# Optimization experiments

Measured on AMD Instinct MI355X. Metric: run time of the kernel, lower is better.

The kernel has to match this reference:

```python
import jax, jax.numpy as jnp
import numpy as np

NEG_SLOPE = 0.2   # GATConv default leaky_relu slope
BN_EPS = 1e-5
N, D, H, DH, E, BS = 49152, 512, 8, 64, 131072, 12
N_LAYERS = 5  # conv6 exists in __init__ but is never called in forward


def setup_inputs() -> dict:
    key = jax.random.key(0)
    ks = jax.random.split(key, 12)
    s = 0.05
    x = jax.random.normal(ks[0], (N, D), jnp.float32)
    edge_index = jax.random.randint(ks[1], (2, E), 0, N, jnp.int64)
    Ws = jax.random.normal(ks[2], (N_LAYERS, D, H * DH), jnp.float32) * s
    Asrc = jax.random.normal(ks[3], (N_LAYERS, H, DH), jnp.float32) * s
    Adst = jax.random.normal(ks[4], (N_LAYERS, H, DH), jnp.float32) * s
    Bconv = jax.random.normal(ks[5], (N_LAYERS, H * DH), jnp.float32) * s
    Gamma = jnp.ones((N_LAYERS, D), jnp.float32)
    Beta = jnp.zeros((N_LAYERS, D), jnp.float32)
    Wl = jax.random.normal(ks[6], (D, 1), jnp.float32) * s
    bl = jnp.zeros((1,), jnp.float32)
    return {"x": x, "edge_index": edge_index, "Ws": Ws, "Asrc": Asrc,
            "Adst": Adst, "Bconv": Bconv, "Gamma": Gamma, "Beta": Beta,
            "Wl": Wl, "bl": bl, "bs": BS}


def _gat_conv(x, src, dst, W, a_src, a_dst, b):
    n = x.shape[0]
    h = (x @ W).reshape(n, H, DH)                      # [N,H,DH]
    al_s = jnp.einsum('nhd,hd->nh', h, a_src)          # [N,H]
    al_d = jnp.einsum('nhd,hd->nh', h, a_dst)
    e = jax.nn.leaky_relu(al_s[src] + al_d[dst], NEG_SLOPE)  # [Etot,H]
    # segment softmax over incoming edges of each dst node
    m = jax.ops.segment_max(e, dst, num_segments=n)
    p = jnp.exp(e - m[dst])
    z = jax.ops.segment_sum(p, dst, num_segments=n)
    alpha = p / (z[dst] + 1e-16)
    out = jax.ops.segment_sum(alpha[:, :, None] * h[src], dst, num_segments=n)
    return out.reshape(n, H * DH) + b


def _batch_norm(x, gamma, beta):
    mu = x.mean(0)
    var = x.var(0)  # biased, as torch BN uses for normalization
    return (x - mu) * jax.lax.rsqrt(var + BN_EPS) * gamma + beta


def reference(x, edge_index, Ws, Asrc, Adst, Bconv, Gamma, Beta, Wl, bl, bs):
    n = x.shape[0]
    loops = jnp.arange(n, dtype=edge_index.dtype)      # add_self_loops=True
    src = jnp.concatenate([edge_index[0], loops])
    dst = jnp.concatenate([edge_index[1], loops])
    for i in range(N_LAYERS):
        x = _gat_conv(x, src, dst, Ws[i], Asrc[i], Adst[i], Bconv[i])
        x = jax.nn.relu(_batch_norm(x, Gamma[i], Beta[i]))
    w = x @ Wl + bl                                    # [N,1]
    return w.reshape(bs, -1)
```

## Files before the change

### kernel.cpp

```cpp
#include <hip/hip_runtime.h>
#include <cstdint>

#define N_NODES 49152
#define DIM 512
#define NH 8
#define DHEAD 64
#define NE 131072
#define ETOT (NE + N_NODES)
#define NLAYERS 5
#define AGG_NODES 32
#define AGG_BLOCKS (N_NODES / AGG_NODES)

typedef short short8 __attribute__((ext_vector_type(8)));
typedef float floatx4 __attribute__((ext_vector_type(4)));

__device__ __forceinline__ float bf2f(unsigned short v) {
  union { unsigned int u; float f; } x; x.u = ((unsigned int)v) << 16; return x.f;
}
__device__ __forceinline__ unsigned short f2bf(float f) {
  union { float f; unsigned int u; } x; x.f = f;
  unsigned int r = x.u + 0x7fffu + ((x.u >> 16) & 1u);
  return (unsigned short)(r >> 16);
}
__device__ __forceinline__ void async_load16(const void* g, void* l) {
  __builtin_amdgcn_global_load_lds((const __attribute__((address_space(1))) void*)g,
                                   (__attribute__((address_space(3))) void*)l, 16, 0, 0);
}

__global__ __launch_bounds__(256) void convert_x_r7(const float* __restrict__ xf, unsigned short* __restrict__ xb)
{
  const size_t i = ((size_t)blockIdx.x * 256 + threadIdx.x) * 8;
  const float4 a = *(const float4*)&xf[i];
  const float4 b = *(const float4*)&xf[i + 4];
  unsigned int ov[4];
  ov[0] = (unsigned int)f2bf(a.x) | ((unsigned int)f2bf(a.y) << 16);
  ov[1] = (unsigned int)f2bf(a.z) | ((unsigned int)f2bf(a.w) << 16);
  ov[2] = (unsigned int)f2bf(b.x) | ((unsigned int)f2bf(b.y) << 16);
  ov[3] = (unsigned int)f2bf(b.z) | ((unsigned int)f2bf(b.w) << 16);
  *(uint4*)&xb[i] = *(const uint4*)ov;
}

__global__ void transpose_w_r7(const float* __restrict__ Ws, unsigned short* __restrict__ WT)
{
  __shared__ float tile[32][33];
  const int l  = blockIdx.z;
  const int nt = blockIdx.x * 32, kt = blockIdx.y * 32;
  const int tx = threadIdx.x & 31, ty = threadIdx.x >> 5;
  #pragma unroll
  for (int r = 0; r < 32; r += 8)
    tile[ty + r][tx] = Ws[(size_t)l*DIM*DIM + (size_t)(kt + ty + r)*DIM + nt + tx];
  __syncthreads();
  #pragma unroll
  for (int r = 0; r < 32; r += 8)
    WT[(size_t)l*DIM*DIM + (size_t)(nt + ty + r)*DIM + kt + tx] = f2bf(tile[tx][ty + r]);
}

__global__ void repack_edges_r7(const int* __restrict__ raw, int* __restrict__ eidx)
{
  const int i = blockIdx.x * 256 + threadIdx.x;
  bool is64 = true;
  #pragma unroll
  for (int j = 0; j < 16; j++) is64 = is64 && (raw[2*j + 1] == 0);
  int v;
  if (is64) v = (int)((const long long*)raw)[i];
  else      v = raw[i];
  eidx[i] = v;
}

__global__ void init_counts_r7(int* __restrict__ counts) {
  counts[blockIdx.x * 256 + threadIdx.x] = 1;
}
__global__ void hist_dst_r7(const int* __restrict__ eidx, int* __restrict__ counts) {
  const int i = blockIdx.x * 256 + threadIdx.x;
  atomicAdd(&counts[eidx[NE + i]], 1);
}
__global__ void scan_kernel_r7(const int* __restrict__ counts, int* __restrict__ offs, int* __restrict__ cursor)
{
  __shared__ int tot[1024];
  const int t = threadIdx.x;
  const int base = t * 48;
  int s = 0;
  for (int i = 0; i < 48; i++) s += counts[base + i];
  tot[t] = s;
  __syncthreads();
  for (int o = 1; o < 1024; o <<= 1) {
    int v = (t >= o) ? tot[t - o] : 0;
    __syncthreads();
    tot[t] += v;
    __syncthreads();
  }
  int run = tot[t] - s;
  for (int i = 0; i < 48; i++) {
    offs[base + i] = run;
    cursor[base + i] = run;
    run += counts[base + i];
  }
  if (t == 1023) offs[N_NODES] = tot[1023];
}
__global__ void scatter_edges_r7(const int* __restrict__ eidx, int* __restrict__ cursor, int* __restrict__ csrc)
{
  const int i = blockIdx.x * 256 + threadIdx.x;
  int s, d;
  if (i < NE) { s = eidx[i]; d = eidx[NE + i]; }
  else        { s = i - NE; d = s; }
  const int pos = atomicAdd(&cursor[d], 1);
  csrc[pos] = s;
}

__global__ __launch_bounds__(512, 4) void gemm_bt_r7(const unsigned short* __restrict__ A,
                                                     const unsigned short* __restrict__ BT,
                                                     const float* __restrict__ asrc,
                                                     const float* __restrict__ adst,
                                                     unsigned short* __restrict__ C,
                                                     float* __restrict__ als,
                                                     float* __restrict__ ald)
{
  __shared__ unsigned short As[128 * 64];
  __shared__ unsigned short Bs[256 * 64];
  const int m0 = blockIdx.x * 128;
  const int n0 = blockIdx.y * 256;
  const int tid = threadIdx.x;
  const int wv = tid >> 6, lane = tid & 63;
  const int wr = (wv & 1) * 64, wc = (wv >> 1) * 64;
  const int q = lane >> 4, c16 = lane & 15;
  const int arow = lane >> 3;
  const int acol = (lane & 7) * 8;

  floatx4 acc[4][4] = {};

  for (int k0 = 0; k0 < DIM; k0 += 64) {
    #pragma unroll
    for (int t = 0; t < 2; t++) {
      const int cb = wv * 2 + t;
      async_load16(A + (size_t)(m0 + cb*8 + arow)*DIM + k0 + acol, &As[cb * 512]);
    }
    #pragma unroll
    for (int t = 0; t < 4; t++) {
      const int cb = wv * 4 + t;
      async_load16(BT + (size_t)(n0 + cb*8 + arow)*DIM + k0 + acol, &Bs[cb * 512]);
    }
    __syncthreads();
    #pragma unroll
    for (int kk = 0; kk < 64; kk += 32) {
      short8 aF[4], bF[4];
      #pragma unroll
      for (int mt = 0; mt < 4; mt++)
        aF[mt] = *(const short8*)&As[(wr + mt*16 + c16) * 64 + kk + q*8];
      #pragma unroll
      for (int nt = 0; nt < 4; nt++)
        bF[nt] = *(const short8*)&Bs[(wc + nt*16 + c16) * 64 + kk + q*8];
      #pragma unroll
      for (int mt = 0; mt < 4; mt++)
        #pragma unroll
        for (int nt = 0; nt < 4; nt++)
          acc[mt][nt] = __builtin_amdgcn_mfma_f32_16x16x32_bf16(aF[mt], bF[nt], acc[mt][nt], 0, 0, 0);
    }
    __syncthreads();
  }
  #pragma unroll
  for (int mt = 0; mt < 4; mt++) {
    #pragma unroll
    for (int nt = 0; nt < 4; nt++) {
      const int col = n0 + wc + nt*16 + c16;
      #pragma unroll
      for (int r = 0; r < 4; r++) {
        const int row = m0 + wr + mt*16 + q*4 + r;
        C[(size_t)row * DIM + col] = f2bf(acc[mt][nt][r]);
      }
    }
  }
  const int head = 4 * blockIdx.y + (wc >> 6);
  float as_[4], ad_[4];
  #pragma unroll
  for (int nt = 0; nt < 4; nt++) {
    const int d = nt * 16 + c16;
    as_[nt] = asrc[head * DHEAD + d];
    ad_[nt] = adst[head * DHEAD + d];
  }
  #pragma unroll
  for (int mt = 0; mt < 4; mt++) {
    #pragma unroll
    for (int r = 0; r < 4; r++) {
      float ss = 0.f, sd = 0.f;
      #pragma unroll
      for (int nt = 0; nt < 4; nt++) {
        ss += acc[mt][nt][r] * as_[nt];
        sd += acc[mt][nt][r] * ad_[nt];
      }
      #pragma unroll
      for (int msk = 1; msk <= 8; msk <<= 1) {
        ss += __shfl_xor(ss, msk, 64);
        sd += __shfl_xor(sd, msk, 64);
      }
      if (c16 == 0) {
        const int row = m0 + wr + mt*16 + q*4 + r;
        als[row * NH + head] = ss;
        ald[row * NH + head] = sd;
      }
    }
  }
}

__global__ __launch_bounds__(256) void gat_agg_r7(const unsigned short* __restrict__ Hm,
    const float* __restrict__ als, const float* __restrict__ ald,
    const int* __restrict__ offs, const int* __restrict__ csrc,
    const float* __restrict__ bconv, unsigned short* __restrict__ Xout,
    float* __restrict__ ps, float* __restrict__ pq)
{
  __shared__ float red[4][1024];
  const int wv = threadIdx.x >> 6, lane = threadIdx.x & 63;
  const int hd = lane >> 3;
  const float4 bA = ((const float4*)(bconv + (size_t)lane * 8))[0];
  const float4 bB = ((const float4*)(bconv + (size_t)lane * 8))[1];
  const float barr[8] = {bA.x, bA.y, bA.z, bA.w, bB.x, bB.y, bB.z, bB.w};
  float cs[8] = {}, cq[8] = {};

  for (int i = 0; i < 8; i++) {
    const int node = blockIdx.x * AGG_NODES + wv * 8 + i;
    const float aldv = ald[node * NH + hd];
    const int e0 = offs[node], e1 = offs[node + 1];
    float m = -1e30f, z = 0.f;
    float acc[8] = {};
    for (int e = e0; e < e1; e++) {
      const int s = csrc[e];
      float lg = als[s * NH + hd] + aldv;
      lg = lg > 0.f ? lg : 0.2f * lg;
      const float mn = fmaxf(m, lg);
      const float sf = __expf(m - mn);
      const float w  = __expf(lg - mn);
      z = z * sf + w;
      const uint4 hv = *(const uint4*)&Hm[(size_t)s * DIM + lane * 8];
      const unsigned int* hp = (const unsigned int*)&hv;
      #pragma unroll
      for (int j = 0; j < 4; j++) {
        acc[2*j]   = acc[2*j]   * sf + w * bf2f((unsigned short)(hp[j] & 0xffffu));
        acc[2*j+1] = acc[2*j+1] * sf + w * bf2f((unsigned short)(hp[j] >> 16));
      }
      m = mn;
    }
    const float zinv = 1.f / (z + 1e-16f);
    unsigned int ov[4];
    #pragma unroll
    for (int j = 0; j < 4; j++) {
      const unsigned short b0 = f2bf(acc[2*j] * zinv + barr[2*j]);
      const unsigned short b1 = f2bf(acc[2*j+1] * zinv + barr[2*j+1]);
      ov[j] = (unsigned int)b0 | ((unsigned int)b1 << 16);
      const float y0 = bf2f(b0), y1 = bf2f(b1);
      cs[2*j]   += y0; cq[2*j]   += y0 * y0;
      cs[2*j+1] += y1; cq[2*j+1] += y1 * y1;
    }
    *(uint4*)&Xout[(size_t)node * DIM + lane * 8] = *(const uint4*)ov;
  }
  #pragma unroll
  for (int j = 0; j < 8; j++) {
    red[wv][lane * 8 + j] = cs[j];
    red[wv][512 + lane * 8 + j] = cq[j];
  }
  __syncthreads();
  const int t = threadIdx.x;
  #pragma unroll
  for (int r = 0; r < 2; r++) {
    const int c = t + r * 256;
    ps[(size_t)blockIdx.x * 512 + c] = red[0][c] + red[1][c] + red[2][c] + red[3][c];
    pq[(size_t)blockIdx.x * 512 + c] = red[0][512+c] + red[1][512+c] + red[2][512+c] + red[3][512+c];
  }
}

__global__ __launch_bounds__(256) void bn_reduce_r7(const float* __restrict__ ps, const float* __restrict__ pq,
                                                    const float* __restrict__ gamma, const float* __restrict__ beta,
                                                    float* __restrict__ scale, float* __restrict__ shift)
{
  __shared__ float rs[256], rq[256];
  const int c = blockIdx.x;
  const int t = threadIdx.x;
  float s = 0.f, q = 0.f;
  for (int b = t; b < AGG_BLOCKS; b += 256) {
    s += ps[(size_t)b * 512 + c];
    q += pq[(size_t)b * 512 + c];
  }
  rs[t] = s; rq[t] = q;
  __syncthreads();
  for (int o = 128; o > 0; o >>= 1) {
    if (t < o) { rs[t] += rs[t + o]; rq[t] += rq[t + o]; }
    __syncthreads();
  }
  if (t == 0) {
    const float inv = 1.0f / (float)N_NODES;
    const float mean = rs[0] * inv;
    float var = rq[0] * inv - mean * mean;
    var = fmaxf(var, 0.f);
    const float rsq = rsqrtf(var + 1e-5f);
    const float sc = gamma[c] * rsq;
    scale[c] = sc;
    shift[c] = beta[c] - mean * sc;
  }
}

__global__ __launch_bounds__(256) void bn_apply_r7(unsigned short* __restrict__ X,
    const float* __restrict__ scale, const float* __restrict__ shift)
{
  const size_t i = ((size_t)blockIdx.x * 256 + threadIdx.x) * 8;
  const int c = (int)(i & (DIM - 1));
  uint4 v = *(const uint4*)&X[i];
  unsigned int* vp = (unsigned int*)&v;
  unsigned int ov[4];
  #pragma unroll
  for (int j = 0; j < 4; j++) {
    const float a = bf2f((unsigned short)(vp[j] & 0xffffu));
    const float b = bf2f((unsigned short)(vp[j] >> 16));
    const float ya = fmaxf(0.f, a * scale[c + 2*j]     + shift[c + 2*j]);
    const float yb = fmaxf(0.f, b * scale[c + 2*j + 1] + shift[c + 2*j + 1]);
    ov[j] = (unsigned int)f2bf(ya) | ((unsigned int)f2bf(yb) << 16);
  }
  *(uint4*)&X[i] = *(const uint4*)ov;
}

__global__ __launch_bounds__(256) void final_head_r7(const unsigned short* __restrict__ X,
    const float* __restrict__ scale, const float* __restrict__ shift,
    const float* __restrict__ wl, const float* __restrict__ blp,
    float* __restrict__ out)
{
  const int wv = threadIdx.x >> 6, lane = threadIdx.x & 63;
  const int node = blockIdx.x * 4 + wv;
  const uint4 xv = *(const uint4*)&X[(size_t)node * DIM + lane * 8];
  const unsigned int* xp = (const unsigned int*)&xv;
  const int c0 = lane * 8;
  float s = 0.f;
  #pragma unroll
  for (int i = 0; i < 4; i++) {
    const float a0 = bf2f((unsigned short)(xp[i] & 0xffffu));
    const float a1 = bf2f((unsigned short)(xp[i] >> 16));
    const float y0 = fmaxf(0.f, a0 * scale[c0 + 2*i]     + shift[c0 + 2*i]);
    const float y1 = fmaxf(0.f, a1 * scale[c0 + 2*i + 1] + shift[c0 + 2*i + 1]);
    s += y0 * wl[c0 + 2*i] + y1 * wl[c0 + 2*i + 1];
  }
  #pragma unroll
  for (int msk = 32; msk >= 1; msk >>= 1) s += __shfl_xor(s, msk, 64);
  if (lane == 0) out[node] = s + blp[0];
}

extern "C" void kernel_launch(void* const* d_in, const int* in_sizes, int n_in,
                              void* d_out, int out_size, void* d_ws, size_t ws_size,
                              hipStream_t stream)
{
  const float* x_in  = (const float*)d_in[0];
  const int*   ei    = (const int*)d_in[1];
  const float* Ws    = (const float*)d_in[2];
  const float* Asrc  = (const float*)d_in[3];
  const float* Adst  = (const float*)d_in[4];
  const float* Bconv = (const float*)d_in[5];
  const float* Gamma = (const float*)d_in[6];
  const float* Beta  = (const float*)d_in[7];
  const float* Wl    = (const float*)d_in[8];
  const float* bl    = (const float*)d_in[9];
  float* out = (float*)d_out;

  char* ws = (char*)d_ws;
  size_t off = 0;
  auto alloc = [&](size_t b) { char* p = ws + off; off += (b + 255) & ~(size_t)255; return p; };
  unsigned short* xbuf = (unsigned short*)alloc((size_t)N_NODES * DIM * 2);
  unsigned short* hbuf = (unsigned short*)alloc((size_t)N_NODES * DIM * 2);
  unsigned short* WT   = (unsigned short*)alloc((size_t)NLAYERS * DIM * DIM * 2);
  float* als   = (float*)alloc((size_t)N_NODES * NH * 4);
  float* ald   = (float*)alloc((size_t)N_NODES * NH * 4);
  int* eidx    = (int*)alloc((size_t)2 * NE * 4);
  int* counts  = (int*)alloc((size_t)N_NODES * 4);
  int* offs    = (int*)alloc(((size_t)N_NODES + 1) * 4);
  int* cursor  = (int*)alloc((size_t)N_NODES * 4);
  int* csrc    = (int*)alloc((size_t)ETOT * 4);
  float* ps    = (float*)alloc((size_t)AGG_BLOCKS * 512 * 4);
  float* pq    = (float*)alloc((size_t)AGG_BLOCKS * 512 * 4);
  float* scale = (float*)alloc(512 * 4);
  float* shift = (float*)alloc(512 * 4);

  convert_x_r7<<<(N_NODES * DIM / 8) / 256, 256, 0, stream>>>(x_in, xbuf);
  transpose_w_r7<<<dim3(16, 16, 5), 256, 0, stream>>>(Ws, WT);
  repack_edges_r7<<<(2 * NE) / 256, 256, 0, stream>>>(ei, eidx);
  init_counts_r7<<<N_NODES / 256, 256, 0, stream>>>(counts);
  hist_dst_r7<<<NE / 256, 256, 0, stream>>>(eidx, counts);
  scan_kernel_r7<<<1, 1024, 0, stream>>>(counts, offs, cursor);
  scatter_edges_r7<<<ETOT / 256, 256, 0, stream>>>(eidx, cursor, csrc);

  for (int l = 0; l < NLAYERS; l++) {
    gemm_bt_r7<<<dim3(N_NODES / 128, DIM / 256), 512, 0, stream>>>(
        xbuf, WT + (size_t)l * DIM * DIM,
        Asrc + l * NH * DHEAD, Adst + l * NH * DHEAD, hbuf, als, ald);
    gat_agg_r7<<<AGG_BLOCKS, 256, 0, stream>>>(hbuf, als, ald, offs, csrc,
                                               Bconv + l * DIM, xbuf, ps, pq);
    bn_reduce_r7<<<512, 256, 0, stream>>>(ps, pq, Gamma + l * DIM, Beta + l * DIM, scale, shift);
    if (l < NLAYERS - 1)
      bn_apply_r7<<<(N_NODES * DIM / 8) / 256, 256, 0, stream>>>(xbuf, scale, shift);
  }
  final_head_r7<<<N_NODES / 4, 256, 0, stream>>>(xbuf, scale, shift, Wl, bl, out);
}
```

Measured before the change: 813.5 us.

## Parallelize GAT edge softmax across lanes and prefetch neighbor rows

For nodes with at most 64 incoming edges, the aggregation kernel now loads all source indices at once, computes the attention logits for all edges in parallel across lane slots, and does a two-pass max/sum softmax with wave shuffles. This replaces the serial online-softmax loop. It then accumulates neighbor feature rows using the precomputed weights and software-prefetches the next row. This aims to remove the serial dependent-load chain and the per-edge exp rescaling, at the cost of more shuffles and register use. Higher-degree nodes keep the old online-softmax path.

```diff
diff --git a/kernel.cpp b/kernel.cpp
--- a/kernel.cpp
+++ b/kernel.cpp
@@ -27,7 +27,7 @@
                                    (__attribute__((address_space(3))) void*)l, 16, 0, 0);
 }
 
-__global__ __launch_bounds__(256) void convert_x_r7(const float* __restrict__ xf, unsigned short* __restrict__ xb)
+__global__ __launch_bounds__(256) void convert_x_r8(const float* __restrict__ xf, unsigned short* __restrict__ xb)
 {
   const size_t i = ((size_t)blockIdx.x * 256 + threadIdx.x) * 8;
   const float4 a = *(const float4*)&xf[i];
@@ -40,7 +40,7 @@
   *(uint4*)&xb[i] = *(const uint4*)ov;
 }
 
-__global__ void transpose_w_r7(const float* __restrict__ Ws, unsigned short* __restrict__ WT)
+__global__ void transpose_w_r8(const float* __restrict__ Ws, unsigned short* __restrict__ WT)
 {
   __shared__ float tile[32][33];
   const int l  = blockIdx.z;
@@ -55,7 +55,7 @@
     WT[(size_t)l*DIM*DIM + (size_t)(nt + ty + r)*DIM + kt + tx] = f2bf(tile[tx][ty + r]);
 }
 
-__global__ void repack_edges_r7(const int* __restrict__ raw, int* __restrict__ eidx)
+__global__ void repack_edges_r8(const int* __restrict__ raw, int* __restrict__ eidx)
 {
   const int i = blockIdx.x * 256 + threadIdx.x;
   bool is64 = true;
@@ -67,14 +67,14 @@
   eidx[i] = v;
 }
 
-__global__ void init_counts_r7(int* __restrict__ counts) {
+__global__ void init_counts_r8(int* __restrict__ counts) {
   counts[blockIdx.x * 256 + threadIdx.x] = 1;
 }
-__global__ void hist_dst_r7(const int* __restrict__ eidx, int* __restrict__ counts) {
+__global__ void hist_dst_r8(const int* __restrict__ eidx, int* __restrict__ counts) {
   const int i = blockIdx.x * 256 + threadIdx.x;
   atomicAdd(&counts[eidx[NE + i]], 1);
 }
-__global__ void scan_kernel_r7(const int* __restrict__ counts, int* __restrict__ offs, int* __restrict__ cursor)
+__global__ void scan_kernel_r8(const int* __restrict__ counts, int* __restrict__ offs, int* __restrict__ cursor)
 {
   __shared__ int tot[1024];
   const int t = threadIdx.x;
@@ -97,7 +97,7 @@
   }
   if (t == 1023) offs[N_NODES] = tot[1023];
 }
-__global__ void scatter_edges_r7(const int* __restrict__ eidx, int* __restrict__ cursor, int* __restrict__ csrc)
+__global__ void scatter_edges_r8(const int* __restrict__ eidx, int* __restrict__ cursor, int* __restrict__ csrc)
 {
   const int i = blockIdx.x * 256 + threadIdx.x;
   int s, d;
@@ -107,7 +107,7 @@
   csrc[pos] = s;
 }
 
-__global__ __launch_bounds__(512, 4) void gemm_bt_r7(const unsigned short* __restrict__ A,
+__global__ __launch_bounds__(512, 4) void gemm_bt_r8(const unsigned short* __restrict__ A,
                                                      const unsigned short* __restrict__ BT,
                                                      const float* __restrict__ asrc,
                                                      const float* __restrict__ adst,
@@ -201,7 +201,7 @@
   }
 }
 
-__global__ __launch_bounds__(256) void gat_agg_r7(const unsigned short* __restrict__ Hm,
+__global__ __launch_bounds__(256) void gat_agg_r8(const unsigned short* __restrict__ Hm,
     const float* __restrict__ als, const float* __restrict__ ald,
     const int* __restrict__ offs, const int* __restrict__ csrc,
     const float* __restrict__ bconv, unsigned short* __restrict__ Xout,
@@ -210,6 +210,8 @@
   __shared__ float red[4][1024];
   const int wv = threadIdx.x >> 6, lane = threadIdx.x & 63;
   const int hd = lane >> 3;
+  const int hp = lane & 7;
+  const int slot = lane >> 3;
   const float4 bA = ((const float4*)(bconv + (size_t)lane * 8))[0];
   const float4 bB = ((const float4*)(bconv + (size_t)lane * 8))[1];
   const float barr[8] = {bA.x, bA.y, bA.z, bA.w, bB.x, bB.y, bB.z, bB.w};
@@ -217,28 +219,93 @@
 
   for (int i = 0; i < 8; i++) {
     const int node = blockIdx.x * AGG_NODES + wv * 8 + i;
-    const float aldv = ald[node * NH + hd];
     const int e0 = offs[node], e1 = offs[node + 1];
-    float m = -1e30f, z = 0.f;
+    const int deg = e1 - e0;
     float acc[8] = {};
-    for (int e = e0; e < e1; e++) {
-      const int s = csrc[e];
-      float lg = als[s * NH + hd] + aldv;
-      lg = lg > 0.f ? lg : 0.2f * lg;
-      const float mn = fmaxf(m, lg);
-      const float sf = __expf(m - mn);
-      const float w  = __expf(lg - mn);
-      z = z * sf + w;
-      const uint4 hv = *(const uint4*)&Hm[(size_t)s * DIM + lane * 8];
-      const unsigned int* hp = (const unsigned int*)&hv;
-      #pragma unroll
-      for (int j = 0; j < 4; j++) {
-        acc[2*j]   = acc[2*j]   * sf + w * bf2f((unsigned short)(hp[j] & 0xffffu));
-        acc[2*j+1] = acc[2*j+1] * sf + w * bf2f((unsigned short)(hp[j] >> 16));
-      }
-      m = mn;
-    }
-    const float zinv = 1.f / (z + 1e-16f);
+    float zinv;
+
+    if (deg <= 64) {
+      const float aldp = ald[node * NH + hp];
+      const int myS = (lane < deg) ? csrc[e0 + lane] : 0;
+      const int nr = (deg + 7) >> 3;
+      float lgsto[8];
+      #pragma unroll
+      for (int r = 0; r < 8; r++) {
+        if (r < nr) {
+          const int k = r * 8 + slot;
+          const int s = __shfl(myS, k & 63, 64);
+          float lg = als[s * NH + hp] + aldp;
+          lg = lg > 0.f ? lg : 0.2f * lg;
+          lgsto[r] = (k < deg) ? lg : -1e30f;
+        } else lgsto[r] = -1e30f;
+      }
+      float m = lgsto[0];
+      #pragma unroll
+      for (int r = 1; r < 8; r++) m = fmaxf(m, lgsto[r]);
+      m = fmaxf(m, __shfl_xor(m, 8, 64));
+      m = fmaxf(m, __shfl_xor(m, 16, 64));
+      m = fmaxf(m, __shfl_xor(m, 32, 64));
+      float z = 0.f;
+      float wsto[8];
+      #pragma unroll
+      for (int r = 0; r < 8; r++) {
+        if (r < nr) {
+          const float w = __expf(lgsto[r] - m);
+          wsto[r] = w; z += w;
+        } else wsto[r] = 0.f;
+      }
+      z += __shfl_xor(z, 8, 64);
+      z += __shfl_xor(z, 16, 64);
+      z += __shfl_xor(z, 32, 64);
+      const float zden = __shfl(z, hd, 64);
+      zinv = 1.f / (zden + 1e-16f);
+
+      int sn = __shfl(myS, 0, 64);
+      uint4 hv = *(const uint4*)&Hm[(size_t)sn * DIM + lane * 8];
+      #pragma unroll
+      for (int r = 0; r < 8; r++) {
+        if (r * 8 < deg) {
+          const int kmax = (deg - r * 8 < 8) ? (deg - r * 8) : 8;
+          for (int kk = 0; kk < kmax; kk++) {
+            const uint4 hcur = hv;
+            const int k = r * 8 + kk;
+            if (k + 1 < deg) {
+              const int s2 = __shfl(myS, (k + 1) & 63, 64);
+              hv = *(const uint4*)&Hm[(size_t)s2 * DIM + lane * 8];
+            }
+            const float w = __shfl(wsto[r], (kk << 3) + hd, 64);
+            const unsigned int* hpx = (const unsigned int*)&hcur;
+            #pragma unroll
+            for (int j = 0; j < 4; j++) {
+              acc[2*j]   += w * bf2f((unsigned short)(hpx[j] & 0xffffu));
+              acc[2*j+1] += w * bf2f((unsigned short)(hpx[j] >> 16));
+            }
+          }
+        }
+      }
+    } else {
+      const float aldv = ald[node * NH + hd];
+      float m = -1e30f, z = 0.f;
+      for (int e = e0; e < e1; e++) {
+        const int s = csrc[e];
+        float lg = als[s * NH + hd] + aldv;
+        lg = lg > 0.f ? lg : 0.2f * lg;
+        const float mn = fmaxf(m, lg);
+        const float sf = __expf(m - mn);
+        const float w  = __expf(lg - mn);
+        z = z * sf + w;
+        const uint4 hv = *(const uint4*)&Hm[(size_t)s * DIM + lane * 8];
+        const unsigned int* hpx = (const unsigned int*)&hv;
+        #pragma unroll
+        for (int j = 0; j < 4; j++) {
+          acc[2*j]   = acc[2*j]   * sf + w * bf2f((unsigned short)(hpx[j] & 0xffffu));
+          acc[2*j+1] = acc[2*j+1] * sf + w * bf2f((unsigned short)(hpx[j] >> 16));
+        }
+        m = mn;
+      }
+      zinv = 1.f / (z + 1e-16f);
+    }
+
     unsigned int ov[4];
     #pragma unroll
     for (int j = 0; j < 4; j++) {
@@ -266,7 +333,7 @@
   }
 }
 
-__global__ __launch_bounds__(256) void bn_reduce_r7(const float* __restrict__ ps, const float* __restrict__ pq,
+__global__ __launch_bounds__(256) void bn_reduce_r8(const float* __restrict__ ps, const float* __restrict__ pq,
                                                     const float* __restrict__ gamma, const float* __restrict__ beta,
                                                     float* __restrict__ scale, float* __restrict__ shift)
 {
@@ -296,7 +363,7 @@
   }
 }
 
-__global__ __launch_bounds__(256) void bn_apply_r7(unsigned short* __restrict__ X,
+__global__ __launch_bounds__(256) void bn_apply_r8(unsigned short* __restrict__ X,
     const float* __restrict__ scale, const float* __restrict__ shift)
 {
   const size_t i = ((size_t)blockIdx.x * 256 + threadIdx.x) * 8;
@@ -315,7 +382,7 @@
   *(uint4*)&X[i] = *(const uint4*)ov;
 }
 
-__global__ __launch_bounds__(256) void final_head_r7(const unsigned short* __restrict__ X,
+__global__ __launch_bounds__(256) void final_head_r8(const unsigned short* __restrict__ X,
     const float* __restrict__ scale, const float* __restrict__ shift,
     const float* __restrict__ wl, const float* __restrict__ blp,
     float* __restrict__ out)
@@ -373,23 +440,23 @@
   float* scale = (float*)alloc(512 * 4);
   float* shift = (float*)alloc(512 * 4);
 
-  convert_x_r7<<<(N_NODES * DIM / 8) / 256, 256, 0, stream>>>(x_in, xbuf);
-  transpose_w_r7<<<dim3(16, 16, 5), 256, 0, stream>>>(Ws, WT);
-  repack_edges_r7<<<(2 * NE) / 256, 256, 0, stream>>>(ei, eidx);
-  init_counts_r7<<<N_NODES / 256, 256, 0, stream>>>(counts);
-  hist_dst_r7<<<NE / 256, 256, 0, stream>>>(eidx, counts);
-  scan_kernel_r7<<<1, 1024, 0, stream>>>(counts, offs, cursor);
-  scatter_edges_r7<<<ETOT / 256, 256, 0, stream>>>(eidx, cursor, csrc);
+  convert_x_r8<<<(N_NODES * DIM / 8) / 256, 256, 0, stream>>>(x_in, xbuf);
+  transpose_w_r8<<<dim3(16, 16, 5), 256, 0, stream>>>(Ws, WT);
+  repack_edges_r8<<<(2 * NE) / 256, 256, 0, stream>>>(ei, eidx);
+  init_counts_r8<<<N_NODES / 256, 256, 0, stream>>>(counts);
+  hist_dst_r8<<<NE / 256, 256, 0, stream>>>(eidx, counts);
+  scan_kernel_r8<<<1, 1024, 0, stream>>>(counts, offs, cursor);
+  scatter_edges_r8<<<ETOT / 256, 256, 0, stream>>>(eidx, cursor, csrc);
 
   for (int l = 0; l < NLAYERS; l++) {
-    gemm_bt_r7<<<dim3(N_NODES / 128, DIM / 256), 512, 0, stream>>>(
+    gemm_bt_r8<<<dim3(N_NODES / 128, DIM / 256), 512, 0, stream>>>(
         xbuf, WT + (size_t)l * DIM * DIM,
         Asrc + l * NH * DHEAD, Adst + l * NH * DHEAD, hbuf, als, ald);
-    gat_agg_r7<<<AGG_BLOCKS, 256, 0, stream>>>(hbuf, als, ald, offs, csrc,
+    gat_agg_r8<<<AGG_BLOCKS, 256, 0, stream>>>(hbuf, als, ald, offs, csrc,
                                                Bconv + l * DIM, xbuf, ps, pq);
-    bn_reduce_r7<<<512, 256, 0, stream>>>(ps, pq, Gamma + l * DIM, Beta + l * DIM, scale, shift);
+    bn_reduce_r8<<<512, 256, 0, stream>>>(ps, pq, Gamma + l * DIM, Beta + l * DIM, scale, shift);
     if (l < NLAYERS - 1)
-      bn_apply_r7<<<(N_NODES * DIM / 8) / 256, 256, 0, stream>>>(xbuf, scale, shift);
-  }
-  final_head_r7<<<N_NODES / 4, 256, 0, stream>>>(xbuf, scale, shift, Wl, bl, out);
-}
+      bn_apply_r8<<<(N_NODES * DIM / 8) / 256, 256, 0, stream>>>(xbuf, scale, shift);
+  }
+  final_head_r8<<<N_NODES / 4, 256, 0, stream>>>(xbuf, scale, shift, Wl, bl, out);
+}
```

After: 881.3 us. 1.08x slower.
